# Kernel tuning notes

Hardware: AMD Instinct MI355X
Metric: run time of the kernel (lower is better)

Reference implementation:

```python
import jax, jax.numpy as jnp
import numpy as np

NUM_HEADS = 12
HEAD_DIM = 64


def setup_inputs() -> dict:
    key = jax.random.key(0)
    ks = jax.random.split(key, 7)
    B, S, D = 32, 577, 768
    scale = 0.02
    return {
        "hidden_states": jax.random.normal(ks[0], (B, S, D), dtype=jnp.float32),
        "Wq": jax.random.normal(ks[1], (D, D), dtype=jnp.float32) * scale,
        "bq": jnp.zeros((D,), dtype=jnp.float32),
        "Wk": jax.random.normal(ks[2], (D, D), dtype=jnp.float32) * scale,
        "bk": jnp.zeros((D,), dtype=jnp.float32),
        "Wv": jax.random.normal(ks[3], (D, D), dtype=jnp.float32) * scale,
        "bv": jnp.zeros((D,), dtype=jnp.float32),
    }


def _split_heads(x):
    # [B, S, D] -> [B, H, S, d]
    B, S, D = x.shape
    return x.reshape(B, S, NUM_HEADS, HEAD_DIM).transpose(0, 2, 1, 3)


def reference(hidden_states, Wq, bq, Wk, bk, Wv, bv):
    # QKV projections (nn.Linear: x @ W.T + b)
    q = _split_heads(hidden_states @ Wq.T + bq)  # [B,H,S,d]
    k = _split_heads(hidden_states @ Wk.T + bk)
    v = _split_heads(hidden_states @ Wv.T + bv)

    inv_scale = 1.0 / np.sqrt(HEAD_DIM).astype(np.float32)
    scores = jnp.einsum("bhqd,bhkd->bhqk", q, k) * inv_scale  # [B,H,S,S]
    probs = jax.nn.softmax(scores, axis=-1)
    ctx = jnp.einsum("bhqk,bhkd->bhqd", probs, v)  # [B,H,S,d]

    B, H, S, d = ctx.shape
    return ctx.transpose(0, 2, 1, 3).reshape(B, S, H * d)  # [B,S,D]
```

## Files before the change

### kernel.cpp

```cpp
#include <hip/hip_runtime.h>


#define SEQ 577
#define DMODEL 768
#define NHEADS 12
#define HDIM 64
#define MTOTAL (32 * 577)
#define MPAD 18560
#define KP 608
#define STW 616

typedef __attribute__((ext_vector_type(8))) short bf16x8;
typedef __attribute__((ext_vector_type(4))) float f32x4;

#define MFMA_BF16(a, b, c) __builtin_amdgcn_mfma_f32_16x16x32_bf16((a), (b), (c), 0, 0, 0)

static __device__ __forceinline__ unsigned short f2bf(float x) {
    unsigned int u = __float_as_uint(x);
    return (unsigned short)((u + 0x7FFFu + ((u >> 16) & 1u)) >> 16);
}
static __device__ __forceinline__ float bf2f(unsigned short s) {
    return __uint_as_float((unsigned int)s << 16);
}
static __device__ __forceinline__ void cvt8(unsigned short* dst, const float* src) {
    float4 a = *reinterpret_cast<const float4*>(src);
    float4 b = *reinterpret_cast<const float4*>(src + 4);
    union { unsigned short us[8]; int4 v; } u;
    u.us[0] = f2bf(a.x); u.us[1] = f2bf(a.y); u.us[2] = f2bf(a.z); u.us[3] = f2bf(a.w);
    u.us[4] = f2bf(b.x); u.us[5] = f2bf(b.y); u.us[6] = f2bf(b.z); u.us[7] = f2bf(b.w);
    *reinterpret_cast<int4*>(dst) = u.v;
}
static __device__ __forceinline__ void gload_lds16(const void* g, void* l) {
    __builtin_amdgcn_global_load_lds(
        (const __attribute__((address_space(1))) void*)g,
        (__attribute__((address_space(3))) void*)l, 16, 0, 0);
}

#define NX8 (MTOTAL * DMODEL / 8)
#define NW8 (DMODEL * DMODEL / 8)
__global__ __launch_bounds__(256) void conv_kernel(
    const float* __restrict__ X, const float* __restrict__ Wq,
    const float* __restrict__ Wk, const float* __restrict__ Wv,
    unsigned short* __restrict__ Xb, unsigned short* __restrict__ Wb)
{
    const int total = NX8 + 3 * NW8;
    for (int i = blockIdx.x * blockDim.x + threadIdx.x; i < total;
         i += gridDim.x * blockDim.x) {
        if (i < NX8) {
            cvt8(Xb + (size_t)i * 8, X + (size_t)i * 8);
        } else {
            int j = i - NX8;
            int w = j / NW8, o = j - w * NW8;
            const float* Wf = (w == 0) ? Wq : ((w == 1) ? Wk : Wv);
            cvt8(Wb + (size_t)w * DMODEL * DMODEL + (size_t)o * 8, Wf + (size_t)o * 8);
        }
    }
}

template<bool FAST>
__global__ __launch_bounds__(256) void gemm_qkv(
    const float* __restrict__ X, const unsigned short* __restrict__ Xb,
    const float* __restrict__ Wq, const float* __restrict__ Wk,
    const float* __restrict__ Wv, const unsigned short* __restrict__ Wb,
    const float* __restrict__ bq, const float* __restrict__ bk,
    const float* __restrict__ bv,
    unsigned short* __restrict__ Qb, unsigned short* __restrict__ Kb,
    unsigned short* __restrict__ Vt, int vstride)
{
    constexpr int LDA = FAST ? 64 : 72;
    __shared__ __align__(16) unsigned short As[128 * LDA];
    __shared__ __align__(16) unsigned short Bs[128 * LDA];

    const int z = blockIdx.z;
    const float* bias = (z == 0) ? bq : ((z == 1) ? bk : bv);
    const float outscale = (z == 0) ? 0.125f : 1.0f;

    const int m0 = blockIdx.x * 128;
    const int n0 = blockIdx.y * 128;
    const int t = (int)threadIdx.x;
    const int lane = t & 63, wid = t >> 6;
    const int hi = lane >> 4, l15 = lane & 15;
    const int wr = wid >> 1, wc = wid & 1;

    const f32x4 zero = {0.f, 0.f, 0.f, 0.f};
    f32x4 acc[4][4];
    #pragma unroll
    for (int i = 0; i < 4; ++i)
        #pragma unroll
        for (int j = 0; j < 4; ++j) acc[i][j] = zero;

    const unsigned short* gA = nullptr; const unsigned short* gB = nullptr;
    const float* xp = nullptr; const float* wp = nullptr;
    if constexpr (FAST) {
        const int srow = wid * 8 + (lane >> 3);
        const int scol = (lane & 7) * 8;
        gA = Xb + (size_t)(m0 + srow) * DMODEL + scol;
        gB = Wb + (size_t)z * DMODEL * DMODEL + (size_t)(n0 + srow) * DMODEL + scol;
    } else {
        const int lrow = t >> 1, lcol = (t & 1) * 32;
        int xr = m0 + lrow; if (xr > MTOTAL - 1) xr = MTOTAL - 1;
        xp = X + (size_t)xr * DMODEL + lcol;
        const float* Wf = (z == 0) ? Wq : ((z == 1) ? Wk : Wv);
        wp = Wf + (size_t)(n0 + lrow) * DMODEL + lcol;
    }

    for (int k0 = 0; k0 < DMODEL; k0 += 64) {
        if constexpr (FAST) {
            #pragma unroll
            for (int c = 0; c < 4; ++c) {
                gload_lds16(gA + (size_t)c * 32 * DMODEL + k0, As + wid * 512 + c * 2048);
                gload_lds16(gB + (size_t)c * 32 * DMODEL + k0, Bs + wid * 512 + c * 2048);
            }
        } else {
            const int lrow = t >> 1, lcol = (t & 1) * 32;
            #pragma unroll
            for (int c = 0; c < 4; ++c) {
                cvt8(As + lrow * LDA + lcol + c * 8, xp + k0 + c * 8);
                cvt8(Bs + lrow * LDA + lcol + c * 8, wp + k0 + c * 8);
            }
        }
        __syncthreads();
        #pragma unroll
        for (int kc = 0; kc < 2; ++kc) {
            bf16x8 a[4], b[4];
            #pragma unroll
            for (int i = 0; i < 4; ++i)
                a[i] = *reinterpret_cast<const bf16x8*>(
                    As + (wr * 64 + i * 16 + l15) * LDA + kc * 32 + hi * 8);
            #pragma unroll
            for (int i = 0; i < 4; ++i)
                b[i] = *reinterpret_cast<const bf16x8*>(
                    Bs + (wc * 64 + i * 16 + l15) * LDA + kc * 32 + hi * 8);
            #pragma unroll
            for (int mf = 0; mf < 4; ++mf)
                #pragma unroll
                for (int nf = 0; nf < 4; ++nf)
                    acc[mf][nf] = MFMA_BF16(a[mf], b[nf], acc[mf][nf]);
        }
        __syncthreads();
    }

    #pragma unroll
    for (int nf = 0; nf < 4; ++nf) {
        const int n = n0 + wc * 64 + nf * 16 + l15;
        const float bval = bias[n];
        const int h = n >> 6, dd = n & 63;
        #pragma unroll
        for (int mf = 0; mf < 4; ++mf) {
            #pragma unroll
            for (int r = 0; r < 4; ++r) {
                const int gm = m0 + wr * 64 + mf * 16 + hi * 4 + r;
                if (gm < MTOTAL) {
                    const int bi = gm / SEQ, s = gm - ((gm / SEQ) * SEQ);
                    const int bh = bi * NHEADS + h;
                    const unsigned short v = f2bf((acc[mf][nf][r] + bval) * outscale);
                    if (z == 2)
                        Vt[((size_t)bh * HDIM + dd) * vstride + s] = v;
                    else if (z == 0)
                        Qb[((size_t)bh * SEQ + s) * HDIM + dd] = v;
                    else
                        Kb[((size_t)bh * SEQ + s) * HDIM + dd] = v;
                }
            }
        }
    }
}

__global__ __launch_bounds__(256) void attn2(
    const unsigned short* __restrict__ Qb,
    const unsigned short* __restrict__ Kb,
    const unsigned short* __restrict__ Vt,
    float* __restrict__ Out, int vstride)
{
    __shared__ __align__(16) unsigned short St[32 * STW];
    __shared__ float rowinv[32];

    const int qt = blockIdx.x, bh = blockIdx.y;
    const int s0 = qt * 32;
    const int t = (int)threadIdx.x;
    const int lane = t & 63, wid = t >> 6;
    const int hi = lane >> 4, l15 = lane & 15;
    const size_t base = (size_t)bh * SEQ * HDIM;
    const f32x4 zero = {0.f, 0.f, 0.f, 0.f};

    bf16x8 qf0[2], qf1[2];
    #pragma unroll
    for (int mb = 0; mb < 2; ++mb) {
        int qrow = s0 + mb * 16 + l15; if (qrow > SEQ - 1) qrow = SEQ - 1;
        const unsigned short* qp = Qb + base + (size_t)qrow * HDIM + hi * 8;
        qf0[mb] = *reinterpret_cast<const bf16x8*>(qp);
        qf1[mb] = *reinterpret_cast<const bf16x8*>(qp + 32);
    }

    for (int kt = wid; kt < 37; kt += 4) {
        int kr = kt * 16 + l15; if (kr > SEQ - 1) kr = SEQ - 1;
        const unsigned short* kp = Kb + base + (size_t)kr * HDIM + hi * 8;
        bf16x8 a0 = *reinterpret_cast<const bf16x8*>(kp);
        bf16x8 a1 = *reinterpret_cast<const bf16x8*>(kp + 32);
        f32x4 acc0 = zero, acc1 = zero;
        acc0 = MFMA_BF16(a0, qf0[0], acc0);
        acc0 = MFMA_BF16(a1, qf1[0], acc0);
        acc1 = MFMA_BF16(a0, qf0[1], acc1);
        acc1 = MFMA_BF16(a1, qf1[1], acc1);
        const int obase = 32 * kt + 8 * hi;
        {
            char* rowp = (char*)St + l15 * (STW * 2);
            int2 w = {(int)((unsigned int)f2bf(acc0[0]) | ((unsigned int)f2bf(acc0[1]) << 16)),
                      (int)((unsigned int)f2bf(acc0[2]) | ((unsigned int)f2bf(acc0[3]) << 16))};
            *reinterpret_cast<int2*>(rowp + obase) = w;
        }
        {
            char* rowp = (char*)St + (16 + l15) * (STW * 2);
            int2 w = {(int)((unsigned int)f2bf(acc1[0]) | ((unsigned int)f2bf(acc1[1]) << 16)),
                      (int)((unsigned int)f2bf(acc1[2]) | ((unsigned int)f2bf(acc1[3]) << 16))};
            *reinterpret_cast<int2*>(rowp + obase) = w;
        }
    }
    __syncthreads();

    {
        const int r = t >> 3, j = t & 7;
        char* rowp = (char*)St + r * (STW * 2);
        float mx = -1e30f;
        for (int cc = j; cc < 74; cc += 8) {
            bf16x8 v = *reinterpret_cast<const bf16x8*>(rowp + cc * 16);
            #pragma unroll
            for (int e = 0; e < 8; ++e) mx = fmaxf(mx, bf2f((unsigned short)v[e]));
        }
        mx = fmaxf(mx, __shfl_xor(mx, 1));
        mx = fmaxf(mx, __shfl_xor(mx, 2));
        mx = fmaxf(mx, __shfl_xor(mx, 4));
        float sum = 0.f;
        for (int cc = j; cc < 74; cc += 8) {
            bf16x8 v = *reinterpret_cast<const bf16x8*>(rowp + cc * 16);
            unsigned int w[4];
            #pragma unroll
            for (int e = 0; e < 8; e += 2) {
                float p0 = __expf(bf2f((unsigned short)v[e]) - mx);
                float p1 = __expf(bf2f((unsigned short)v[e + 1]) - mx);
                if (cc * 8 + e     >= SEQ) p0 = 0.f;
                if (cc * 8 + e + 1 >= SEQ) p1 = 0.f;
                sum += p0 + p1;
                w[e >> 1] = (unsigned int)f2bf(p0) | ((unsigned int)f2bf(p1) << 16);
            }
            int4 wv = {(int)w[0], (int)w[1], (int)w[2], (int)w[3]};
            *reinterpret_cast<int4*>(rowp + cc * 16) = wv;
        }
        if (j < 2) {
            int4 zv = {0, 0, 0, 0};
            *reinterpret_cast<int4*>(rowp + (74 + j) * 16) = zv;
        }
        sum += __shfl_xor(sum, 1);
        sum += __shfl_xor(sum, 2);
        sum += __shfl_xor(sum, 4);
        if (j == 0) rowinv[r] = 1.0f / sum;
    }
    __syncthreads();

    f32x4 o0 = zero, o1 = zero;
    const int dd = wid * 16 + l15;
    const unsigned short* vbase = Vt + ((size_t)bh * HDIM + dd) * vstride;
    for (int k0 = 0; k0 < KP; k0 += 32) {
        int vk = k0 + hi * 8;
        if (vk > 576) vk = 576;
        union { bf16x8 v8; int2 d2[2]; } u;
        u.d2[0] = *reinterpret_cast<const int2*>(vbase + vk);
        u.d2[1] = *reinterpret_cast<const int2*>(vbase + vk + 4);
        #pragma unroll
        for (int mb = 0; mb < 2; ++mb) {
            const int q = mb * 16 + l15;
            const char* pp = (const char*)St + q * (STW * 2) + 2 * k0 + 16 * hi;
            bf16x8 pa = *reinterpret_cast<const bf16x8*>(pp);
            if (mb == 0) o0 = MFMA_BF16(pa, u.v8, o0);
            else         o1 = MFMA_BF16(pa, u.v8, o1);
        }
    }

    const int bi = bh / NHEADS, h = bh - bi * NHEADS;
    #pragma unroll
    for (int r = 0; r < 4; ++r) {
        {
            const int q = hi * 4 + r, s = s0 + q;
            if (s < SEQ)
                Out[((size_t)bi * SEQ + s) * DMODEL + h * HDIM + dd] = o0[r] * rowinv[q];
        }
        {
            const int q = 16 + hi * 4 + r, s = s0 + q;
            if (s < SEQ)
                Out[((size_t)bi * SEQ + s) * DMODEL + h * HDIM + dd] = o1[r] * rowinv[q];
        }
    }
}

extern "C" void kernel_launch(void* const* d_in, const int* in_sizes, int n_in,
                              void* d_out, int out_size, void* d_ws, size_t ws_size,
                              hipStream_t stream) {
    (void)in_sizes; (void)n_in; (void)out_size;
    const float* X  = (const float*)d_in[0];
    const float* Wq = (const float*)d_in[1];
    const float* bq = (const float*)d_in[2];
    const float* Wk = (const float*)d_in[3];
    const float* bk = (const float*)d_in[4];
    const float* Wv = (const float*)d_in[5];
    const float* bv = (const float*)d_in[6];
    float* Out = (float*)d_out;

    const size_t E_QK = (size_t)MTOTAL * DMODEL;
    const size_t E_XB = (size_t)MPAD * DMODEL;
    const size_t E_WB = 3ull * DMODEL * DMODEL;
    const size_t E_VT_F = 384ull * HDIM * KP;
    const size_t need_fast = (E_XB + E_WB + 2 * E_QK + E_VT_F) * 2;

    const bool fast = (ws_size >= need_fast);
    unsigned short* p = (unsigned short*)d_ws;
    unsigned short *Xb = nullptr, *Wb = nullptr, *Qb, *Kb, *Vt;
    int vstride;
    if (fast) {
        Xb = p; p += E_XB;
        Wb = p; p += E_WB;
        Qb = p; p += E_QK;
        Kb = p; p += E_QK;
        Vt = p;
        vstride = KP;
    } else {
        Qb = p; p += E_QK;
        Kb = p; p += E_QK;
        Vt = p;
        vstride = 584;
    }

    dim3 gg((MPAD) / 128, DMODEL / 128, 3);
    if (fast) {
        conv_kernel<<<2048, 256, 0, stream>>>(X, Wq, Wk, Wv, Xb, Wb);
        gemm_qkv<true><<<gg, 256, 0, stream>>>(X, Xb, Wq, Wk, Wv, Wb,
                                               bq, bk, bv, Qb, Kb, Vt, vstride);
    } else {
        gemm_qkv<false><<<gg, 256, 0, stream>>>(X, Xb, Wq, Wk, Wv, Wb,
                                                bq, bk, bv, Qb, Kb, Vt, vstride);
    }
    attn2<<<dim3((SEQ + 31) / 32, 32 * NHEADS), 256, 0, stream>>>(Qb, Kb, Vt, Out, vstride);
}
```

Measured before the change: 426.5 us.

## Double-buffer QKV GEMM LDS tiles with XOR swizzle and prefetch K/V in attention

The fast QKV GEMM path now uses two LDS buffers, issuing the next k-step's global-to-LDS loads before computing the current one, with manual vmcnt waits and raw barriers. It also applies an XOR swizzle to the LDS column layout to reduce bank conflicts. The attention kernel software-prefetches the next K tile in the score loop and the next V fragment in the PV loop, with the first V load issued before softmax, and raises wave priority during the PV MFMA loop. LDS use doubles for the GEMM, which may reduce occupancy, and the manual waitcnt logic depends on the exact count of outstanding loads.

```diff
diff --git a/kernel.cpp b/kernel.cpp
--- a/kernel.cpp
+++ b/kernel.cpp
@@ -5,10 +5,11 @@
 #define DMODEL 768
 #define NHEADS 12
 #define HDIM 64
-#define MTOTAL (32 * 577)
+#define MTOTAL (32 * SEQ)
 #define MPAD 18560
 #define KP 608
 #define STW 616
+#define NKSTEP (DMODEL / 64)
 
 typedef __attribute__((ext_vector_type(8))) short bf16x8;
 typedef __attribute__((ext_vector_type(4))) float f32x4;
@@ -67,9 +68,8 @@
     unsigned short* __restrict__ Qb, unsigned short* __restrict__ Kb,
     unsigned short* __restrict__ Vt, int vstride)
 {
-    constexpr int LDA = FAST ? 64 : 72;
-    __shared__ __align__(16) unsigned short As[128 * LDA];
-    __shared__ __align__(16) unsigned short Bs[128 * LDA];
+    __shared__ __align__(16) unsigned short As[FAST ? 2 * 128 * 64 : 128 * 72];
+    __shared__ __align__(16) unsigned short Bs[FAST ? 2 * 128 * 64 : 128 * 72];
 
     const int z = blockIdx.z;
     const float* bias = (z == 0) ? bq : ((z == 1) ? bk : bv);
@@ -89,55 +89,86 @@
         #pragma unroll
         for (int j = 0; j < 4; ++j) acc[i][j] = zero;
 
-    const unsigned short* gA = nullptr; const unsigned short* gB = nullptr;
-    const float* xp = nullptr; const float* wp = nullptr;
     if constexpr (FAST) {
         const int srow = wid * 8 + (lane >> 3);
-        const int scol = (lane & 7) * 8;
-        gA = Xb + (size_t)(m0 + srow) * DMODEL + scol;
-        gB = Wb + (size_t)z * DMODEL * DMODEL + (size_t)(n0 + srow) * DMODEL + scol;
+        const int scol = (((lane & 7) ^ ((lane >> 3) & 7))) * 8;
+        const unsigned short* gA = Xb + (size_t)(m0 + srow) * DMODEL + scol;
+        const unsigned short* gB = Wb + (size_t)z * DMODEL * DMODEL
+                                      + (size_t)(n0 + srow) * DMODEL + scol;
+        #define STAGE(buf, k0)                                                     \
+            {                                                                      \
+                _Pragma("unroll")                                                  \
+                for (int c = 0; c < 4; ++c) {                                      \
+                    gload_lds16(gA + (size_t)c * 32 * DMODEL + (k0),               \
+                                &As[(buf) * 8192 + wid * 512 + c * 2048]);         \
+                    gload_lds16(gB + (size_t)c * 32 * DMODEL + (k0),               \
+                                &Bs[(buf) * 8192 + wid * 512 + c * 2048]);         \
+                }                                                                  \
+            }
+        STAGE(0, 0);
+        int cur = 0;
+        for (int kt = 0; kt < NKSTEP; ++kt) {
+            if (kt + 1 < NKSTEP) {
+                STAGE(cur ^ 1, (kt + 1) * 64);
+                asm volatile("s_waitcnt vmcnt(8)" ::: "memory");
+            } else {
+                asm volatile("s_waitcnt vmcnt(0)" ::: "memory");
+            }
+            __builtin_amdgcn_s_barrier();
+            #pragma unroll
+            for (int kc = 0; kc < 2; ++kc) {
+                const int pc = ((kc * 4 + hi) ^ (l15 & 7)) * 8;
+                bf16x8 a[4], b[4];
+                #pragma unroll
+                for (int i = 0; i < 4; ++i)
+                    a[i] = *reinterpret_cast<const bf16x8*>(
+                        &As[cur * 8192 + (wr * 64 + i * 16 + l15) * 64 + pc]);
+                #pragma unroll
+                for (int i = 0; i < 4; ++i)
+                    b[i] = *reinterpret_cast<const bf16x8*>(
+                        &Bs[cur * 8192 + (wc * 64 + i * 16 + l15) * 64 + pc]);
+                #pragma unroll
+                for (int mf = 0; mf < 4; ++mf)
+                    #pragma unroll
+                    for (int nf = 0; nf < 4; ++nf)
+                        acc[mf][nf] = MFMA_BF16(a[mf], b[nf], acc[mf][nf]);
+            }
+            __builtin_amdgcn_s_barrier();
+            cur ^= 1;
+        }
+        #undef STAGE
     } else {
         const int lrow = t >> 1, lcol = (t & 1) * 32;
         int xr = m0 + lrow; if (xr > MTOTAL - 1) xr = MTOTAL - 1;
-        xp = X + (size_t)xr * DMODEL + lcol;
+        const float* xp = X + (size_t)xr * DMODEL + lcol;
         const float* Wf = (z == 0) ? Wq : ((z == 1) ? Wk : Wv);
-        wp = Wf + (size_t)(n0 + lrow) * DMODEL + lcol;
-    }
-
-    for (int k0 = 0; k0 < DMODEL; k0 += 64) {
-        if constexpr (FAST) {
+        const float* wp = Wf + (size_t)(n0 + lrow) * DMODEL + lcol;
+        for (int k0 = 0; k0 < DMODEL; k0 += 64) {
             #pragma unroll
             for (int c = 0; c < 4; ++c) {
-                gload_lds16(gA + (size_t)c * 32 * DMODEL + k0, As + wid * 512 + c * 2048);
-                gload_lds16(gB + (size_t)c * 32 * DMODEL + k0, Bs + wid * 512 + c * 2048);
-            }
-        } else {
-            const int lrow = t >> 1, lcol = (t & 1) * 32;
-            #pragma unroll
-            for (int c = 0; c < 4; ++c) {
-                cvt8(As + lrow * LDA + lcol + c * 8, xp + k0 + c * 8);
-                cvt8(Bs + lrow * LDA + lcol + c * 8, wp + k0 + c * 8);
-            }
-        }
-        __syncthreads();
-        #pragma unroll
-        for (int kc = 0; kc < 2; ++kc) {
-            bf16x8 a[4], b[4];
-            #pragma unroll
-            for (int i = 0; i < 4; ++i)
-                a[i] = *reinterpret_cast<const bf16x8*>(
-                    As + (wr * 64 + i * 16 + l15) * LDA + kc * 32 + hi * 8);
-            #pragma unroll
-            for (int i = 0; i < 4; ++i)
-                b[i] = *reinterpret_cast<const bf16x8*>(
-                    Bs + (wc * 64 + i * 16 + l15) * LDA + kc * 32 + hi * 8);
-            #pragma unroll
-            for (int mf = 0; mf < 4; ++mf)
-                #pragma unroll
-                for (int nf = 0; nf < 4; ++nf)
-                    acc[mf][nf] = MFMA_BF16(a[mf], b[nf], acc[mf][nf]);
-        }
-        __syncthreads();
+                cvt8(&As[lrow * 72 + lcol + c * 8], xp + k0 + c * 8);
+                cvt8(&Bs[lrow * 72 + lcol + c * 8], wp + k0 + c * 8);
+            }
+            __syncthreads();
+            #pragma unroll
+            for (int kc = 0; kc < 2; ++kc) {
+                bf16x8 a[4], b[4];
+                #pragma unroll
+                for (int i = 0; i < 4; ++i)
+                    a[i] = *reinterpret_cast<const bf16x8*>(
+                        &As[(wr * 64 + i * 16 + l15) * 72 + kc * 32 + hi * 8]);
+                #pragma unroll
+                for (int i = 0; i < 4; ++i)
+                    b[i] = *reinterpret_cast<const bf16x8*>(
+                        &Bs[(wc * 64 + i * 16 + l15) * 72 + kc * 32 + hi * 8]);
+                #pragma unroll
+                for (int mf = 0; mf < 4; ++mf)
+                    #pragma unroll
+                    for (int nf = 0; nf < 4; ++nf)
+                        acc[mf][nf] = MFMA_BF16(a[mf], b[nf], acc[mf][nf]);
+            }
+            __syncthreads();
+        }
     }
 
     #pragma unroll
@@ -192,16 +223,26 @@
         qf1[mb] = *reinterpret_cast<const bf16x8*>(qp + 32);
     }
 
+    bf16x8 kb0, kb1;
+    {
+        int kr = wid * 16 + l15; if (kr > SEQ - 1) kr = SEQ - 1;
+        const unsigned short* kp = Kb + base + (size_t)kr * HDIM + hi * 8;
+        kb0 = *reinterpret_cast<const bf16x8*>(kp);
+        kb1 = *reinterpret_cast<const bf16x8*>(kp + 32);
+    }
     for (int kt = wid; kt < 37; kt += 4) {
-        int kr = kt * 16 + l15; if (kr > SEQ - 1) kr = SEQ - 1;
-        const unsigned short* kp = Kb + base + (size_t)kr * HDIM + hi * 8;
-        bf16x8 a0 = *reinterpret_cast<const bf16x8*>(kp);
-        bf16x8 a1 = *reinterpret_cast<const bf16x8*>(kp + 32);
+        bf16x8 nb0 = kb0, nb1 = kb1;
+        if (kt + 4 < 37) {
+            int kr = (kt + 4) * 16 + l15; if (kr > SEQ - 1) kr = SEQ - 1;
+            const unsigned short* kp = Kb + base + (size_t)kr * HDIM + hi * 8;
+            nb0 = *reinterpret_cast<const bf16x8*>(kp);
+            nb1 = *reinterpret_cast<const bf16x8*>(kp + 32);
+        }
         f32x4 acc0 = zero, acc1 = zero;
-        acc0 = MFMA_BF16(a0, qf0[0], acc0);
-        acc0 = MFMA_BF16(a1, qf1[0], acc0);
-        acc1 = MFMA_BF16(a0, qf0[1], acc1);
-        acc1 = MFMA_BF16(a1, qf1[1], acc1);
+        acc0 = MFMA_BF16(kb0, qf0[0], acc0);
+        acc0 = MFMA_BF16(kb1, qf1[0], acc0);
+        acc1 = MFMA_BF16(kb0, qf0[1], acc1);
+        acc1 = MFMA_BF16(kb1, qf1[1], acc1);
         const int obase = 32 * kt + 8 * hi;
         {
             char* rowp = (char*)St + l15 * (STW * 2);
@@ -215,8 +256,20 @@
                       (int)((unsigned int)f2bf(acc1[2]) | ((unsigned int)f2bf(acc1[3]) << 16))};
             *reinterpret_cast<int2*>(rowp + obase) = w;
         }
+        kb0 = nb0; kb1 = nb1;
     }
     __syncthreads();
+
+    const int dd = wid * 16 + l15;
+    const unsigned short* vbase = Vt + ((size_t)bh * HDIM + dd) * vstride;
+    bf16x8 vcur;
+    {
+        int vk = hi * 8; if (vk > 576) vk = 576;
+        union { bf16x8 v8; int2 d2[2]; } u;
+        u.d2[0] = *reinterpret_cast<const int2*>(vbase + vk);
+        u.d2[1] = *reinterpret_cast<const int2*>(vbase + vk + 4);
+        vcur = u.v8;
+    }
 
     {
         const int r = t >> 3, j = t & 7;
@@ -258,23 +311,24 @@
     __syncthreads();
 
     f32x4 o0 = zero, o1 = zero;
-    const int dd = wid * 16 + l15;
-    const unsigned short* vbase = Vt + ((size_t)bh * HDIM + dd) * vstride;
+    __builtin_amdgcn_s_setprio(1);
     for (int k0 = 0; k0 < KP; k0 += 32) {
-        int vk = k0 + hi * 8;
-        if (vk > 576) vk = 576;
-        union { bf16x8 v8; int2 d2[2]; } u;
-        u.d2[0] = *reinterpret_cast<const int2*>(vbase + vk);
-        u.d2[1] = *reinterpret_cast<const int2*>(vbase + vk + 4);
-        #pragma unroll
-        for (int mb = 0; mb < 2; ++mb) {
-            const int q = mb * 16 + l15;
-            const char* pp = (const char*)St + q * (STW * 2) + 2 * k0 + 16 * hi;
-            bf16x8 pa = *reinterpret_cast<const bf16x8*>(pp);
-            if (mb == 0) o0 = MFMA_BF16(pa, u.v8, o0);
-            else         o1 = MFMA_BF16(pa, u.v8, o1);
-        }
-    }
+        bf16x8 vnext = vcur;
+        if (k0 + 32 < KP) {
+            int vk = k0 + 32 + hi * 8; if (vk > 576) vk = 576;
+            union { bf16x8 v8; int2 d2[2]; } u;
+            u.d2[0] = *reinterpret_cast<const int2*>(vbase + vk);
+            u.d2[1] = *reinterpret_cast<const int2*>(vbase + vk + 4);
+            vnext = u.v8;
+        }
+        const char* pbase = (const char*)St + 2 * k0 + 16 * hi;
+        bf16x8 pa0 = *reinterpret_cast<const bf16x8*>(pbase + l15 * (STW * 2));
+        bf16x8 pa1 = *reinterpret_cast<const bf16x8*>(pbase + (16 + l15) * (STW * 2));
+        o0 = MFMA_BF16(pa0, vcur, o0);
+        o1 = MFMA_BF16(pa1, vcur, o1);
+        vcur = vnext;
+    }
+    __builtin_amdgcn_s_setprio(0);
 
     const int bi = bh / NHEADS, h = bh - bi * NHEADS;
     #pragma unroll
```

Measured after the change: 418.2 us. 2.0% less time.
